# Kernel tuning notes

Hardware: AMD Instinct MI355X
Metric: run time of the kernel (lower is better)

## Reference

```python
import jax, jax.numpy as jnp
import numpy as np

N, E = 50000, 800000
D, H, C, ED = 128, 8, 16, 4  # embed_dim, heads, head_dim, edge_dim


def _add_self_loops(edge_index, ea, n):
    # PyG add_self_loops with fill_value='mean': self-loop edge_attr is the
    # mean of incoming edge attributes per destination node (0 if none).
    src, dst = edge_index[0], edge_index[1]
    deg = jax.ops.segment_sum(jnp.ones((src.shape[0],), ea.dtype), dst, num_segments=n)
    loop_ea = jax.ops.segment_sum(ea, dst, num_segments=n) / jnp.maximum(deg, 1.0)[:, None]
    ar = jnp.arange(n, dtype=src.dtype)
    return (jnp.concatenate([src, ar]), jnp.concatenate([dst, ar]),
            jnp.concatenate([ea, loop_ea], axis=0))


def _gatv2(x, src, dst, ea, Wl, bl, Wr, br, We, att, bias, concat):
    n = x.shape[0]
    xl = (x @ Wl + bl).reshape(n, H, C)   # lin_l -> messages (source)
    xr = (x @ Wr + br).reshape(n, H, C)   # lin_r -> target
    e = (ea @ We).reshape(-1, H, C)       # lin_edge (no bias in PyG)
    m = jax.nn.leaky_relu(xl[src] + xr[dst] + e, negative_slope=0.2)  # [Etot,H,C]
    alpha = jnp.einsum('ehc,hc->eh', m, att)
    amax = jax.ops.segment_max(alpha, dst, num_segments=n)   # every node has a self loop
    ex = jnp.exp(alpha - amax[dst])
    den = jax.ops.segment_sum(ex, dst, num_segments=n)
    a = ex / den[dst]                                        # segment softmax over dst
    out = jax.ops.segment_sum(xl[src] * a[:, :, None], dst, num_segments=n)  # [N,H,C]
    out = out.reshape(n, H * C) if concat else out.mean(axis=1)
    return out + bias


def _ln(h, g, b):
    mu = h.mean(-1, keepdims=True)
    var = jnp.var(h, axis=-1, keepdims=True)
    return (h - mu) / jnp.sqrt(var + 1e-5) * g + b


def setup_inputs() -> dict:
    key = jax.random.key(0)
    ks = jax.random.split(key, 32)
    s = 0.05
    inp = {
        'x': jax.random.normal(ks[0], (N, D), jnp.float32),
        'edge_index': jax.random.randint(ks[1], (2, E), 0, N, jnp.int32),
        'edge_attr': jax.random.normal(ks[2], (E, ED), jnp.float32),
    }
    dims = [(D, H * C), (H * C, H * C), (H * C, C)]  # (in_dim, bias_dim per layer)
    k = 3
    for i, (din, bdim) in enumerate(dims):
        inp[f'Wl{i}'] = jax.random.normal(ks[k], (din, H * C), jnp.float32) * s; k += 1
        inp[f'bl{i}'] = jnp.zeros((H * C,), jnp.float32)
        inp[f'Wr{i}'] = jax.random.normal(ks[k], (din, H * C), jnp.float32) * s; k += 1
        inp[f'br{i}'] = jnp.zeros((H * C,), jnp.float32)
        inp[f'We{i}'] = jax.random.normal(ks[k], (ED, H * C), jnp.float32) * s; k += 1
        inp[f'att{i}'] = jax.random.normal(ks[k], (H, C), jnp.float32) * s; k += 1
        inp[f'b{i}'] = jnp.zeros((bdim,), jnp.float32)
        inp[f'g{i}'] = jnp.ones((bdim,), jnp.float32)
        inp[f'be{i}'] = jnp.zeros((bdim,), jnp.float32)
    inp['Wout'] = jax.random.normal(ks[k], (C, D), jnp.float32) * s
    inp['bout'] = jnp.zeros((D,), jnp.float32)
    return inp


def reference(x, edge_index, edge_attr,
              Wl0, bl0, Wr0, br0, We0, att0, b0, g0, be0,
              Wl1, bl1, Wr1, br1, We1, att1, b1, g1, be1,
              Wl2, bl2, Wr2, br2, We2, att2, b2, g2, be2,
              Wout, bout):
    n = x.shape[0]
    src, dst, ea = _add_self_loops(edge_index, edge_attr, n)
    layers = [
        (Wl0, bl0, Wr0, br0, We0, att0, b0, g0, be0, True),
        (Wl1, bl1, Wr1, br1, We1, att1, b1, g1, be1, True),
        (Wl2, bl2, Wr2, br2, We2, att2, b2, g2, be2, False),
    ]
    for (Wl, bl, Wr, br, We, att, bias, g, be, concat) in layers:
        h = _gatv2(x, src, dst, ea, Wl, bl, Wr, br, We, att, bias, concat)
        h = jax.nn.elu(h)
        h = _ln(h, g, be)
        if h.shape == x.shape:  # residual (layers 0,1)
            h = h + x
        x = h
    return x @ Wout + bout
```

## Files before the change

kernel.cpp:

```cpp
#include <hip/hip_runtime.h>
#include <hip/hip_bf16.h>

#define ND 128
#define NH 8
#define NC 16

typedef float v2f __attribute__((ext_vector_type(2)));

static inline size_t alignup(size_t x){ return (x + 255) & ~size_t(255); }

__device__ __forceinline__ ushort f2bf(float f){
    __hip_bfloat16 h = __float2bfloat16(f);
    return *reinterpret_cast<ushort*>(&h);
}

__device__ __forceinline__ v2f unpack_bf2(uint u){
    v2f r;
    r.x = __uint_as_float(u << 16);
    r.y = __uint_as_float(u & 0xffff0000u);
    return r;
}

__device__ __forceinline__ v2f lrelu2(v2f z){
    v2f s = z * 0.2f;
    v2f r;
    r.x = fmaxf(z.x, s.x);
    r.y = fmaxf(z.y, s.y);
    return r;
}

__device__ __forceinline__ float hred8(float x){
    int y;
    y = __builtin_amdgcn_mov_dpp(__float_as_int(x), 0xB1, 0xF, 0xF, true);
    x += __int_as_float(y);
    y = __builtin_amdgcn_mov_dpp(__float_as_int(x), 0x4E, 0xF, 0xF, true);
    x += __int_as_float(y);
    y = __builtin_amdgcn_mov_dpp(__float_as_int(x), 0x141, 0xF, 0xF, true);
    x += __int_as_float(y);
    return x;
}


__global__ void hist_kernel(const int* __restrict__ dsts, int* __restrict__ deg, int E)
{
    int e = blockIdx.x * blockDim.x + threadIdx.x;
    if (e >= E) return;
    atomicAdd(&deg[dsts[e]], 1);
}

__global__ __launch_bounds__(1024) void scan_kernel(const int* __restrict__ deg,
                                                    int* __restrict__ rowstart, int n)
{
    __shared__ int wsum[16];
    int tid = threadIdx.x;
    int lane = tid & 63, wid = tid >> 6;
    int carry = 0;
    for (int base = 0; base < n; base += 1024) {
        int idx = base + tid;
        int v = (idx < n) ? ((deg[idx] + 3) & ~3) : 0;
        int s = v;
        #pragma unroll
        for (int o = 1; o < 64; o <<= 1) {
            int t = __shfl_up(s, o);
            if (lane >= o) s += t;
        }
        if (lane == 63) wsum[wid] = s;
        __syncthreads();
        int off = 0;
        #pragma unroll
        for (int w = 0; w < 16; ++w) {
            int ws_ = wsum[w];
            if (w < wid) off += ws_;
        }
        int total = 0;
        #pragma unroll
        for (int w = 0; w < 16; ++w) total += wsum[w];
        if (idx < n) rowstart[idx] = carry + off + (s - v);
        carry += total;
        __syncthreads();
    }
    if (tid == 0) rowstart[n] = carry;
}

__global__ void scatter_kernel(const int* __restrict__ srcs, const int* __restrict__ dsts,
                               const float4* __restrict__ ea4,
                               const int* __restrict__ rowstart, int* __restrict__ cursor,
                               int* __restrict__ srcb_sorted, float4* __restrict__ ea_sorted, int E)
{
    int e = blockIdx.x * blockDim.x + threadIdx.x;
    if (e >= E) return;
    int d = dsts[e];
    int pos = rowstart[d] + atomicAdd(&cursor[d], 1);
    srcb_sorted[pos] = srcs[e] << 8;
    ea_sorted[pos] = ea4[e];
}

__global__ void padfill_kernel(const int* __restrict__ rowstart, const int* __restrict__ deg,
                               int* __restrict__ srcb_sorted, float4* __restrict__ ea_sorted, int n)
{
    int v = blockIdx.x * blockDim.x + threadIdx.x;
    if (v < n) {
        int d = deg[v];
        int p = rowstart[v] + d;
        int pe = rowstart[v] + ((d + 3) & ~3);
        for (; p < pe; ++p) {
            srcb_sorted[p] = 0;
            ea_sorted[p] = make_float4(0.f, 0.f, 0.f, 0.f);
        }
    } else if (v < n + 64) {
        int p = rowstart[n] + (v - n);
        srcb_sorted[p] = 0;
        ea_sorted[p] = make_float4(0.f, 0.f, 0.f, 0.f);
    }
}

__global__ void easum_kernel(const int* __restrict__ rowstart, const int* __restrict__ deg,
                             const float4* __restrict__ ea_sorted, float4* __restrict__ easum, int n)
{
    int v = blockIdx.x * blockDim.x + threadIdx.x;
    if (v >= n) return;
    int p0 = rowstart[v], d = deg[v];
    float sx = 0.f, sy = 0.f, sz = 0.f, sw = 0.f;
    for (int p = p0; p < p0 + d; ++p) {
        float4 a = ea_sorted[p];
        sx += a.x; sy += a.y; sz += a.z; sw += a.w;
    }
    float inv = 1.0f / (float)(d > 0 ? d : 1);
    easum[v] = make_float4(sx * inv, sy * inv, sz * inv, sw * inv);
}


__global__ __launch_bounds__(256) void gemm_xw2(const float* __restrict__ X,
                                                const float* __restrict__ Wl,
                                                const float* __restrict__ bl,
                                                const float* __restrict__ Wr,
                                                const float* __restrict__ br,
                                                ushort* __restrict__ XLB,
                                                ushort* __restrict__ XRB, int nrows)
{
    __shared__ float xs[64][128];
    int tid = threadIdx.x;
    int row0 = blockIdx.x * 64;

    const float4* X4 = (const float4*)X;
    float4* xs4 = (float4*)xs;
    #pragma unroll
    for (int i = tid; i < 64*32; i += 256) {
        int r = i >> 5;
        float4 v = make_float4(0.f, 0.f, 0.f, 0.f);
        if (row0 + r < nrows) v = X4[(size_t)(row0 + r) * 32 + (i & 31)];
        xs4[i] = v;
    }
    __syncthreads();

    int cg = tid & 31;
    int rg = (tid >> 5) * 8;
    v2f al0[8], al1[8], ar0[8], ar1[8];
    float4 blv = ((const float4*)bl)[cg];
    float4 brv = ((const float4*)br)[cg];
    #pragma unroll
    for (int r = 0; r < 8; r++) {
        al0[r] = (v2f){blv.x, blv.y}; al1[r] = (v2f){blv.z, blv.w};
        ar0[r] = (v2f){brv.x, brv.y}; ar1[r] = (v2f){brv.z, brv.w};
    }

    #pragma unroll 2
    for (int k = 0; k < 128; k++) {
        float4 wl = ((const float4*)(Wl + (size_t)k * 128))[cg];
        float4 wr = ((const float4*)(Wr + (size_t)k * 128))[cg];
        v2f wl01 = (v2f){wl.x, wl.y}, wl23 = (v2f){wl.z, wl.w};
        v2f wr01 = (v2f){wr.x, wr.y}, wr23 = (v2f){wr.z, wr.w};
        #pragma unroll
        for (int r = 0; r < 8; r++) {
            float xv = xs[rg + r][k];
            v2f xv2 = (v2f){xv, xv};
            al0[r] += xv2 * wl01;
            al1[r] += xv2 * wl23;
            ar0[r] += xv2 * wr01;
            ar1[r] += xv2 * wr23;
        }
    }

    #pragma unroll
    for (int r = 0; r < 8; r++) {
        int row = row0 + rg + r;
        if (row < nrows) {
            ushort4 ol, orr;
            ol.x = f2bf(al0[r].x); ol.y = f2bf(al0[r].y);
            ol.z = f2bf(al1[r].x); ol.w = f2bf(al1[r].y);
            orr.x = f2bf(ar0[r].x); orr.y = f2bf(ar0[r].y);
            orr.z = f2bf(ar1[r].x); orr.w = f2bf(ar1[r].y);
            ((ushort4*)XLB)[(size_t)row * 32 + cg] = ol;
            ((ushort4*)XRB)[(size_t)row * 32 + cg] = orr;
        }
    }
}


__device__ __forceinline__ void gat_wave(
    int dstv, int t,
    const uint* __restrict__ xl_u, const uint* __restrict__ xr_u,
    const int* __restrict__ rowstart, const int* __restrict__ deg,
    const int* __restrict__ srcb_sorted, const float4* __restrict__ ea_sorted,
    const float4* __restrict__ easum,
    const float* __restrict__ We, const float* __restrict__ att,
    v2f& r_out, float& l_out)
{
    v2f we0  = ((const v2f*)(We))[t];
    v2f we1  = ((const v2f*)(We + ND))[t];
    v2f we2  = ((const v2f*)(We + 2*ND))[t];
    v2f we3  = ((const v2f*)(We + 3*ND))[t];
    v2f attv = ((const v2f*)att)[t] * 1.44269504f;
    v2f xrv  = unpack_bf2(xr_u[(((uint)dstv) << 6) + t]);

    int p0 = __builtin_amdgcn_readfirstlane(rowstart[dstv]);
    int dv = __builtin_amdgcn_readfirstlane(deg[dstv]);
    int nb = (dv + 3) >> 2;

    uint xsw = xl_u[(((uint)dstv) << 6) + t];

    const int* sp = srcb_sorted + p0;
    const float4* ep = ea_sorted + p0;
    const char* xlc = (const char*)xl_u;
    uint t4 = (uint)t * 4u;

    v2f a = {0.f, 0.f};
    float lsum = 0.f;

    int4 sA = *(const int4*)(sp);
    uint xA0 = *(const uint*)(xlc + ((uint)sA.x + t4));
    uint xA1 = *(const uint*)(xlc + ((uint)sA.y + t4));
    uint xA2 = *(const uint*)(xlc + ((uint)sA.z + t4));
    uint xA3 = *(const uint*)(xlc + ((uint)sA.w + t4));
    int4 sB = *(const int4*)(sp + 4);
    uint xB0 = *(const uint*)(xlc + ((uint)sB.x + t4));
    uint xB1 = *(const uint*)(xlc + ((uint)sB.y + t4));
    uint xB2 = *(const uint*)(xlc + ((uint)sB.z + t4));
    uint xB3 = *(const uint*)(xlc + ((uint)sB.w + t4));
    int4 sC = *(const int4*)(sp + 8);

    for (int ib = 0; ib < nb; ++ib) {
        uint xC0 = *(const uint*)(xlc + ((uint)sC.x + t4));
        uint xC1 = *(const uint*)(xlc + ((uint)sC.y + t4));
        uint xC2 = *(const uint*)(xlc + ((uint)sC.z + t4));
        uint xC3 = *(const uint*)(xlc + ((uint)sC.w + t4));
        int4 sD = *(const int4*)(sp + ib*4 + 12);
        float4 ea0 = ep[ib*4];
        float4 ea1 = ep[ib*4 + 1];
        float4 ea2 = ep[ib*4 + 2];
        float4 ea3 = ep[ib*4 + 3];

        v2f b0 = xrv + we0*ea0.x + we1*ea0.y + we2*ea0.z + we3*ea0.w;
        v2f b1 = xrv + we0*ea1.x + we1*ea1.y + we2*ea1.z + we3*ea1.w;
        v2f b2 = xrv + we0*ea2.x + we1*ea2.y + we2*ea2.z + we3*ea2.w;
        v2f b3 = xrv + we0*ea3.x + we1*ea3.y + we2*ea3.z + we3*ea3.w;

        v2f x0 = unpack_bf2(xA0);
        v2f x1 = unpack_bf2(xA1);
        v2f x2 = unpack_bf2(xA2);
        v2f x3 = unpack_bf2(xA3);

        v2f l0 = lrelu2(x0 + b0);
        v2f l1 = lrelu2(x1 + b1);
        v2f l2 = lrelu2(x2 + b2);
        v2f l3 = lrelu2(x3 + b3);

        v2f q0 = l0 * attv;
        v2f q1 = l1 * attv;
        v2f q2 = l2 * attv;
        v2f q3 = l3 * attv;
        float pt0 = q0.x + q0.y;
        float pt1 = q1.x + q1.y;
        float pt2 = q2.x + q2.y;
        float pt3 = q3.x + q3.y;

        if (ib == nb - 1) {
            int live = dv - ib*4;
            pt1 = (live > 1) ? pt1 : -1e30f;
            pt2 = (live > 2) ? pt2 : -1e30f;
            pt3 = (live > 3) ? pt3 : -1e30f;
        }

        float al0 = hred8(pt0);
        float al1 = hred8(pt1);
        float al2 = hred8(pt2);
        float al3 = hred8(pt3);

        float pe0 = exp2f(al0);
        float pe1 = exp2f(al1);
        float pe2 = exp2f(al2);
        float pe3 = exp2f(al3);
        lsum += (pe0 + pe1) + (pe2 + pe3);
        a += x0 * pe0;
        a += x1 * pe1;
        a += x2 * pe2;
        a += x3 * pe3;

        xA0 = xB0; xA1 = xB1; xA2 = xB2; xA3 = xB3;
        xB0 = xC0; xB1 = xC1; xB2 = xC2; xB3 = xC3;
        sC = sD;
    }

    float4 em = easum[dstv];
    v2f xs = unpack_bf2(xsw);
    v2f bs = xrv + we0*em.x + we1*em.y + we2*em.z + we3*em.w;
    v2f ls = lrelu2(xs + bs);
    v2f qs = ls * attv;
    float al = hred8(qs.x + qs.y);
    float pe = exp2f(al);
    l_out = lsum + pe;
    r_out = a + xs * pe;
}

__global__ __launch_bounds__(256) void attn_concat(
    const ushort* __restrict__ xlb, const ushort* __restrict__ xrb,
    const float* __restrict__ xin,
    const int* __restrict__ rowstart, const int* __restrict__ deg,
    const int* __restrict__ srcb_sorted, const float4* __restrict__ ea_sorted,
    const float4* __restrict__ easum,
    const float* __restrict__ We, const float* __restrict__ att,
    const float* __restrict__ bias, const float* __restrict__ g, const float* __restrict__ be,
    float* __restrict__ out, int n)
{
    int wid = threadIdx.x >> 6;
    int t = threadIdx.x & 63;
    int dstv = blockIdx.x * 4 + wid;
    if (dstv >= n) return;

    v2f av; float l;
    gat_wave(dstv, t, (const uint*)xlb, (const uint*)xrb, rowstart, deg, srcb_sorted,
             ea_sorted, easum, We, att, av, l);

    v2f bv = ((const v2f*)bias)[t];
    float linv = 1.0f / l;
    v2f h = av * linv + bv;
    h.x = h.x > 0.f ? h.x : (__expf(h.x) - 1.0f);
    h.y = h.y > 0.f ? h.y : (__expf(h.y) - 1.0f);

    float ss = h.x + h.y, qq = h.x*h.x + h.y*h.y;
    #pragma unroll
    for (int o = 1; o < 64; o <<= 1) { ss += __shfl_xor(ss, o); qq += __shfl_xor(qq, o); }
    float mu = ss * (1.0f / ND);
    float var = qq * (1.0f / ND) - mu * mu;
    float rstd = rsqrtf(var + 1e-5f);

    v2f gv  = ((const v2f*)g)[t];
    v2f bev = ((const v2f*)be)[t];
    v2f xiv = ((const v2f*)(xin + (size_t)dstv * ND))[t];
    v2f o2 = (h - mu) * rstd * gv + bev + xiv;
    ((v2f*)(out + (size_t)dstv * ND))[t] = o2;
}

__global__ __launch_bounds__(256) void attn_final(
    const ushort* __restrict__ xlb, const ushort* __restrict__ xrb,
    const int* __restrict__ rowstart, const int* __restrict__ deg,
    const int* __restrict__ srcb_sorted, const float4* __restrict__ ea_sorted,
    const float4* __restrict__ easum,
    const float* __restrict__ We, const float* __restrict__ att,
    const float* __restrict__ b2, const float* __restrict__ g2, const float* __restrict__ be2,
    const float* __restrict__ Wout, const float* __restrict__ bout,
    float* __restrict__ out, int n)
{
    __shared__ float h16s[4][16];
    int wid = threadIdx.x >> 6;
    int t = threadIdx.x & 63;
    int dstv = blockIdx.x * 4 + wid;
    if (dstv >= n) return;

    v2f av; float l;
    gat_wave(dstv, t, (const uint*)xlb, (const uint*)xrb, rowstart, deg, srcb_sorted,
             ea_sorted, easum, We, att, av, l);
    float linv = 1.0f / l;
    float v0 = av.x * linv, v1 = av.y * linv;

    #pragma unroll
    for (int o = 8; o < 64; o <<= 1) { v0 += __shfl_xor(v0, o); v1 += __shfl_xor(v1, o); }
    int cc = t & 7;
    float2 b2v = ((const float2*)b2)[cc];
    v0 = v0 * (1.0f / NH) + b2v.x;
    v1 = v1 * (1.0f / NH) + b2v.y;
    v0 = v0 > 0.f ? v0 : (__expf(v0) - 1.0f);
    v1 = v1 > 0.f ? v1 : (__expf(v1) - 1.0f);

    float ss = v0 + v1, qq = v0*v0 + v1*v1;
    #pragma unroll
    for (int o = 1; o < 8; o <<= 1) { ss += __shfl_xor(ss, o); qq += __shfl_xor(qq, o); }
    float mu = ss * (1.0f / NC);
    float var = qq * (1.0f / NC) - mu * mu;
    float rstd = rsqrtf(var + 1e-5f);
    float2 g2v = ((const float2*)g2)[cc];
    float2 be2v = ((const float2*)be2)[cc];
    float t0 = (v0 - mu) * rstd * g2v.x + be2v.x;
    float t1 = (v1 - mu) * rstd * g2v.y + be2v.y;

    if (t < 8) { h16s[wid][2*t] = t0; h16s[wid][2*t + 1] = t1; }

    float2 ov = ((const float2*)bout)[t];
    #pragma unroll
    for (int k = 0; k < NC; k++) {
        float hk = h16s[wid][k];
        float2 wv = ((const float2*)Wout)[k * 64 + t];
        ov.x = fmaf(hk, wv.x, ov.x);
        ov.y = fmaf(hk, wv.y, ov.y);
    }
    ((float2*)(out + (size_t)dstv * ND))[t] = ov;
}


extern "C" void kernel_launch(void* const* d_in, const int* in_sizes, int n_in,
                              void* d_out, int out_size, void* d_ws, size_t ws_size,
                              hipStream_t stream)
{
    const float* x_in = (const float*)d_in[0];
    const int*   ei   = (const int*)d_in[1];
    const float* ea   = (const float*)d_in[2];
    const int N = in_sizes[0] / ND;
    const int E = in_sizes[1] / 2;
    const int* srcs = ei;
    const int* dsts = ei + E;
    const float4* ea4 = (const float4*)ea;

    const float *Wl[3], *bl[3], *Wr[3], *br[3], *We[3], *att[3], *bb[3], *gg[3], *be[3];
    for (int l = 0; l < 3; l++) {
        int b = 3 + 9 * l;
        Wl[l]  = (const float*)d_in[b + 0];
        bl[l]  = (const float*)d_in[b + 1];
        Wr[l]  = (const float*)d_in[b + 2];
        br[l]  = (const float*)d_in[b + 3];
        We[l]  = (const float*)d_in[b + 4];
        att[l] = (const float*)d_in[b + 5];
        bb[l]  = (const float*)d_in[b + 6];
        gg[l]  = (const float*)d_in[b + 7];
        be[l]  = (const float*)d_in[b + 8];
    }
    const float* Wout = (const float*)d_in[30];
    const float* bout = (const float*)d_in[31];

    const size_t EP = (size_t)E + 3 * (size_t)N + 80;

    char* ws = (char*)d_ws;
    size_t off = 0;
    int* deg        = (int*)(ws + off);      off = alignup(off + (size_t)N * 4);
    int* cursor     = (int*)(ws + off);      off = alignup(off + (size_t)N * 4);
    size_t zero_bytes = off;
    int* rowstart   = (int*)(ws + off);      off = alignup(off + (size_t)(N + 1) * 4);
    int* srcb_sorted = (int*)(ws + off);     off = alignup(off + EP * 4);
    float4* ea_sorted = (float4*)(ws + off); off = alignup(off + EP * 16);
    float4* easum   = (float4*)(ws + off);   off = alignup(off + (size_t)N * 16);
    ushort* xlb     = (ushort*)(ws + off);   off = alignup(off + (size_t)N * ND * 2);
    ushort* xrb     = (ushort*)(ws + off);   off = alignup(off + (size_t)N * ND * 2);
    float* xa       = (float*)(ws + off);    off = alignup(off + (size_t)N * ND * 4);
    float* xb       = (float*)d_out;

    hipMemsetAsync(d_ws, 0, zero_bytes, stream);

    int ethreads = 256;
    int eblocks = (E + ethreads - 1) / ethreads;
    hist_kernel<<<eblocks, ethreads, 0, stream>>>(dsts, deg, E);
    scan_kernel<<<1, 1024, 0, stream>>>(deg, rowstart, N);
    padfill_kernel<<<(N + 64 + 255) / 256, 256, 0, stream>>>(rowstart, deg, srcb_sorted, ea_sorted, N);
    scatter_kernel<<<eblocks, ethreads, 0, stream>>>(srcs, dsts, ea4, rowstart, cursor,
                                                     srcb_sorted, ea_sorted, E);
    easum_kernel<<<(N + 255) / 256, 256, 0, stream>>>(rowstart, deg, ea_sorted, easum, N);

    int gblocks = (N + 63) / 64;
    int ablocks = (N + 3) / 4;

    gemm_xw2<<<gblocks, 256, 0, stream>>>(x_in, Wl[0], bl[0], Wr[0], br[0], xlb, xrb, N);
    attn_concat<<<ablocks, 256, 0, stream>>>(xlb, xrb, x_in, rowstart, deg, srcb_sorted, ea_sorted,
                                             easum, We[0], att[0], bb[0], gg[0], be[0], xa, N);
    gemm_xw2<<<gblocks, 256, 0, stream>>>(xa, Wl[1], bl[1], Wr[1], br[1], xlb, xrb, N);
    attn_concat<<<ablocks, 256, 0, stream>>>(xlb, xrb, xa, rowstart, deg, srcb_sorted, ea_sorted,
                                             easum, We[1], att[1], bb[1], gg[1], be[1], xb, N);
    gemm_xw2<<<gblocks, 256, 0, stream>>>(xb, Wl[2], bl[2], Wr[2], br[2], xlb, xrb, N);
    attn_final<<<ablocks, 256, 0, stream>>>(xlb, xrb, rowstart, deg, srcb_sorted, ea_sorted,
                                            easum, We[2], att[2], bb[2], gg[2], be[2],
                                            Wout, bout, (float*)d_out, N);
}
```

Measured before the change: 480.5 us.

## Store edge attrs as bf16, deepen gather prefetch, stage weights in LDS, vectorize scan

Sorted edge attributes are packed as bf16 pairs (8 bytes instead of 16 per edge), which cuts edge-attribute traffic in the attention kernels and in easum. The attention loop's source-feature prefetch goes from two to three blocks ahead, and edge attributes are loaded one block ahead. The GEMM stages Wl/Wr in LDS in 16-row tiles with register double-buffering instead of reading weights from global memory each k. The scan now handles four elements per thread. The cost is bf16 rounding of edge attributes and higher register pressure in the attention loop.

```diff
diff --git a/kernel.cpp b/kernel.cpp
--- a/kernel.cpp
+++ b/kernel.cpp
@@ -55,10 +55,19 @@
     int tid = threadIdx.x;
     int lane = tid & 63, wid = tid >> 6;
     int carry = 0;
-    for (int base = 0; base < n; base += 1024) {
-        int idx = base + tid;
-        int v = (idx < n) ? ((deg[idx] + 3) & ~3) : 0;
-        int s = v;
+    for (int base = 0; base < n; base += 4096) {
+        int idx = base + tid * 4;
+        int4 d = make_int4(0, 0, 0, 0);
+        if (idx + 3 < n) d = *(const int4*)(deg + idx);
+        else {
+            if (idx < n)     d.x = deg[idx];
+            if (idx + 1 < n) d.y = deg[idx + 1];
+            if (idx + 2 < n) d.z = deg[idx + 2];
+        }
+        int p0 = (d.x + 3) & ~3, p1 = (d.y + 3) & ~3;
+        int p2 = (d.z + 3) & ~3, p3 = (d.w + 3) & ~3;
+        int tsum = p0 + p1 + p2 + p3;
+        int s = tsum;
         #pragma unroll
         for (int o = 1; o < 64; o <<= 1) {
             int t = __shfl_up(s, o);
@@ -66,7 +75,7 @@
         }
         if (lane == 63) wsum[wid] = s;
         __syncthreads();
-        int off = 0;
+        int off = carry;
         #pragma unroll
         for (int w = 0; w < 16; ++w) {
             int ws_ = wsum[w];
@@ -75,7 +84,11 @@
         int total = 0;
         #pragma unroll
         for (int w = 0; w < 16; ++w) total += wsum[w];
-        if (idx < n) rowstart[idx] = carry + off + (s - v);
+        int excl = off + (s - tsum);
+        if (idx < n)     rowstart[idx]     = excl;
+        if (idx + 1 < n) rowstart[idx + 1] = excl + p0;
+        if (idx + 2 < n) rowstart[idx + 2] = excl + p0 + p1;
+        if (idx + 3 < n) rowstart[idx + 3] = excl + p0 + p1 + p2;
         carry += total;
         __syncthreads();
     }
@@ -85,18 +98,22 @@
 __global__ void scatter_kernel(const int* __restrict__ srcs, const int* __restrict__ dsts,
                                const float4* __restrict__ ea4,
                                const int* __restrict__ rowstart, int* __restrict__ cursor,
-                               int* __restrict__ srcb_sorted, float4* __restrict__ ea_sorted, int E)
+                               int* __restrict__ srcb_sorted, uint2* __restrict__ eab_sorted, int E)
 {
     int e = blockIdx.x * blockDim.x + threadIdx.x;
     if (e >= E) return;
     int d = dsts[e];
     int pos = rowstart[d] + atomicAdd(&cursor[d], 1);
     srcb_sorted[pos] = srcs[e] << 8;
-    ea_sorted[pos] = ea4[e];
+    float4 a = ea4[e];
+    uint2 p;
+    p.x = (uint)f2bf(a.x) | ((uint)f2bf(a.y) << 16);
+    p.y = (uint)f2bf(a.z) | ((uint)f2bf(a.w) << 16);
+    eab_sorted[pos] = p;
 }
 
 __global__ void padfill_kernel(const int* __restrict__ rowstart, const int* __restrict__ deg,
-                               int* __restrict__ srcb_sorted, float4* __restrict__ ea_sorted, int n)
+                               int* __restrict__ srcb_sorted, uint2* __restrict__ eab_sorted, int n)
 {
     int v = blockIdx.x * blockDim.x + threadIdx.x;
     if (v < n) {
@@ -105,25 +122,28 @@
         int pe = rowstart[v] + ((d + 3) & ~3);
         for (; p < pe; ++p) {
             srcb_sorted[p] = 0;
-            ea_sorted[p] = make_float4(0.f, 0.f, 0.f, 0.f);
+            eab_sorted[p] = make_uint2(0u, 0u);
         }
     } else if (v < n + 64) {
         int p = rowstart[n] + (v - n);
         srcb_sorted[p] = 0;
-        ea_sorted[p] = make_float4(0.f, 0.f, 0.f, 0.f);
+        eab_sorted[p] = make_uint2(0u, 0u);
     }
 }
 
 __global__ void easum_kernel(const int* __restrict__ rowstart, const int* __restrict__ deg,
-                             const float4* __restrict__ ea_sorted, float4* __restrict__ easum, int n)
+                             const uint2* __restrict__ eab_sorted, float4* __restrict__ easum, int n)
 {
     int v = blockIdx.x * blockDim.x + threadIdx.x;
     if (v >= n) return;
     int p0 = rowstart[v], d = deg[v];
     float sx = 0.f, sy = 0.f, sz = 0.f, sw = 0.f;
     for (int p = p0; p < p0 + d; ++p) {
-        float4 a = ea_sorted[p];
-        sx += a.x; sy += a.y; sz += a.z; sw += a.w;
+        uint2 a = eab_sorted[p];
+        sx += __uint_as_float(a.x << 16);
+        sy += __uint_as_float(a.x & 0xffff0000u);
+        sz += __uint_as_float(a.y << 16);
+        sw += __uint_as_float(a.y & 0xffff0000u);
     }
     float inv = 1.0f / (float)(d > 0 ? d : 1);
     easum[v] = make_float4(sx * inv, sy * inv, sz * inv, sw * inv);
@@ -139,6 +159,8 @@
                                                 ushort* __restrict__ XRB, int nrows)
 {
     __shared__ float xs[64][128];
+    __shared__ float wls[16][128];
+    __shared__ float wrs[16][128];
     int tid = threadIdx.x;
     int row0 = blockIdx.x * 64;
 
@@ -151,7 +173,11 @@
         if (row0 + r < nrows) v = X4[(size_t)(row0 + r) * 32 + (i & 31)];
         xs4[i] = v;
     }
-    __syncthreads();
+
+    const float4* Wl4 = (const float4*)Wl;
+    const float4* Wr4 = (const float4*)Wr;
+    float4 pa0 = Wl4[tid], pa1 = Wl4[tid + 256];
+    float4 pb0 = Wr4[tid], pb1 = Wr4[tid + 256];
 
     int cg = tid & 31;
     int rg = (tid >> 5) * 8;
@@ -164,20 +190,31 @@
         ar0[r] = (v2f){brv.x, brv.y}; ar1[r] = (v2f){brv.z, brv.w};
     }
 
-    #pragma unroll 2
-    for (int k = 0; k < 128; k++) {
-        float4 wl = ((const float4*)(Wl + (size_t)k * 128))[cg];
-        float4 wr = ((const float4*)(Wr + (size_t)k * 128))[cg];
-        v2f wl01 = (v2f){wl.x, wl.y}, wl23 = (v2f){wl.z, wl.w};
-        v2f wr01 = (v2f){wr.x, wr.y}, wr23 = (v2f){wr.z, wr.w};
+    for (int kt = 0; kt < 128; kt += 16) {
+        __syncthreads();
+        ((float4*)wls)[tid] = pa0; ((float4*)wls)[tid + 256] = pa1;
+        ((float4*)wrs)[tid] = pb0; ((float4*)wrs)[tid + 256] = pb1;
+        __syncthreads();
+        if (kt + 16 < 128) {
+            int base = (kt + 16) * 32;
+            pa0 = Wl4[base + tid]; pa1 = Wl4[base + tid + 256];
+            pb0 = Wr4[base + tid]; pb1 = Wr4[base + tid + 256];
+        }
         #pragma unroll
-        for (int r = 0; r < 8; r++) {
-            float xv = xs[rg + r][k];
-            v2f xv2 = (v2f){xv, xv};
-            al0[r] += xv2 * wl01;
-            al1[r] += xv2 * wl23;
-            ar0[r] += xv2 * wr01;
-            ar1[r] += xv2 * wr23;
+        for (int kk = 0; kk < 16; kk++) {
+            float4 wl = ((const float4*)&wls[kk][0])[cg];
+            float4 wr = ((const float4*)&wrs[kk][0])[cg];
+            v2f wl01 = (v2f){wl.x, wl.y}, wl23 = (v2f){wl.z, wl.w};
+            v2f wr01 = (v2f){wr.x, wr.y}, wr23 = (v2f){wr.z, wr.w};
+            #pragma unroll
+            for (int r = 0; r < 8; r++) {
+                float xv = xs[rg + r][kt + kk];
+                v2f xv2 = (v2f){xv, xv};
+                al0[r] += xv2 * wl01;
+                al1[r] += xv2 * wl23;
+                ar0[r] += xv2 * wr01;
+                ar1[r] += xv2 * wr23;
+            }
         }
     }
 
@@ -201,7 +238,7 @@
     int dstv, int t,
     const uint* __restrict__ xl_u, const uint* __restrict__ xr_u,
     const int* __restrict__ rowstart, const int* __restrict__ deg,
-    const int* __restrict__ srcb_sorted, const float4* __restrict__ ea_sorted,
+    const int* __restrict__ srcb_sorted, const uint2* __restrict__ eab_sorted,
     const float4* __restrict__ easum,
     const float* __restrict__ We, const float* __restrict__ att,
     v2f& r_out, float& l_out)
@@ -220,40 +257,54 @@
     uint xsw = xl_u[(((uint)dstv) << 6) + t];
 
     const int* sp = srcb_sorted + p0;
-    const float4* ep = ea_sorted + p0;
+    const uint4* ebp = (const uint4*)(eab_sorted + p0);
     const char* xlc = (const char*)xl_u;
     uint t4 = (uint)t * 4u;
 
     v2f a = {0.f, 0.f};
     float lsum = 0.f;
 
-    int4 sA = *(const int4*)(sp);
-    uint xA0 = *(const uint*)(xlc + ((uint)sA.x + t4));
-    uint xA1 = *(const uint*)(xlc + ((uint)sA.y + t4));
-    uint xA2 = *(const uint*)(xlc + ((uint)sA.z + t4));
-    uint xA3 = *(const uint*)(xlc + ((uint)sA.w + t4));
-    int4 sB = *(const int4*)(sp + 4);
-    uint xB0 = *(const uint*)(xlc + ((uint)sB.x + t4));
-    uint xB1 = *(const uint*)(xlc + ((uint)sB.y + t4));
-    uint xB2 = *(const uint*)(xlc + ((uint)sB.z + t4));
-    uint xB3 = *(const uint*)(xlc + ((uint)sB.w + t4));
-    int4 sC = *(const int4*)(sp + 8);
+    int4 s0 = *(const int4*)(sp);
+    uint xA0 = *(const uint*)(xlc + ((uint)s0.x + t4));
+    uint xA1 = *(const uint*)(xlc + ((uint)s0.y + t4));
+    uint xA2 = *(const uint*)(xlc + ((uint)s0.z + t4));
+    uint xA3 = *(const uint*)(xlc + ((uint)s0.w + t4));
+    int4 s1 = *(const int4*)(sp + 4);
+    uint xB0 = *(const uint*)(xlc + ((uint)s1.x + t4));
+    uint xB1 = *(const uint*)(xlc + ((uint)s1.y + t4));
+    uint xB2 = *(const uint*)(xlc + ((uint)s1.z + t4));
+    uint xB3 = *(const uint*)(xlc + ((uint)s1.w + t4));
+    int4 s2 = *(const int4*)(sp + 8);
+    uint xC0 = *(const uint*)(xlc + ((uint)s2.x + t4));
+    uint xC1 = *(const uint*)(xlc + ((uint)s2.y + t4));
+    uint xC2 = *(const uint*)(xlc + ((uint)s2.z + t4));
+    uint xC3 = *(const uint*)(xlc + ((uint)s2.w + t4));
+    int4 s3 = *(const int4*)(sp + 12);
+    uint4 eA = ebp[0];
+    uint4 eB = ebp[1];
 
     for (int ib = 0; ib < nb; ++ib) {
-        uint xC0 = *(const uint*)(xlc + ((uint)sC.x + t4));
-        uint xC1 = *(const uint*)(xlc + ((uint)sC.y + t4));
-        uint xC2 = *(const uint*)(xlc + ((uint)sC.z + t4));
-        uint xC3 = *(const uint*)(xlc + ((uint)sC.w + t4));
-        int4 sD = *(const int4*)(sp + ib*4 + 12);
-        float4 ea0 = ep[ib*4];
-        float4 ea1 = ep[ib*4 + 1];
-        float4 ea2 = ep[ib*4 + 2];
-        float4 ea3 = ep[ib*4 + 3];
-
-        v2f b0 = xrv + we0*ea0.x + we1*ea0.y + we2*ea0.z + we3*ea0.w;
-        v2f b1 = xrv + we0*ea1.x + we1*ea1.y + we2*ea1.z + we3*ea1.w;
-        v2f b2 = xrv + we0*ea2.x + we1*ea2.y + we2*ea2.z + we3*ea2.w;
-        v2f b3 = xrv + we0*ea3.x + we1*ea3.y + we2*ea3.z + we3*ea3.w;
+        uint xD0 = *(const uint*)(xlc + ((uint)s3.x + t4));
+        uint xD1 = *(const uint*)(xlc + ((uint)s3.y + t4));
+        uint xD2 = *(const uint*)(xlc + ((uint)s3.z + t4));
+        uint xD3 = *(const uint*)(xlc + ((uint)s3.w + t4));
+        int4 s4 = *(const int4*)(sp + ib*4 + 16);
+        uint4 eNA = ebp[(ib + 1) * 2];
+        uint4 eNB = ebp[(ib + 1) * 2 + 1];
+
+        float e0x = __uint_as_float(eA.x << 16), e0y = __uint_as_float(eA.x & 0xffff0000u);
+        float e0z = __uint_as_float(eA.y << 16), e0w = __uint_as_float(eA.y & 0xffff0000u);
+        float e1x = __uint_as_float(eA.z << 16), e1y = __uint_as_float(eA.z & 0xffff0000u);
+        float e1z = __uint_as_float(eA.w << 16), e1w = __uint_as_float(eA.w & 0xffff0000u);
+        float e2x = __uint_as_float(eB.x << 16), e2y = __uint_as_float(eB.x & 0xffff0000u);
+        float e2z = __uint_as_float(eB.y << 16), e2w = __uint_as_float(eB.y & 0xffff0000u);
+        float e3x = __uint_as_float(eB.z << 16), e3y = __uint_as_float(eB.z & 0xffff0000u);
+        float e3z = __uint_as_float(eB.w << 16), e3w = __uint_as_float(eB.w & 0xffff0000u);
+
+        v2f b0 = xrv + we0*e0x + we1*e0y + we2*e0z + we3*e0w;
+        v2f b1 = xrv + we0*e1x + we1*e1y + we2*e1z + we3*e1w;
+        v2f b2 = xrv + we0*e2x + we1*e2y + we2*e2z + we3*e2w;
+        v2f b3 = xrv + we0*e3x + we1*e3y + we2*e3z + we3*e3w;
 
         v2f x0 = unpack_bf2(xA0);
         v2f x1 = unpack_bf2(xA1);
@@ -298,7 +349,9 @@
 
         xA0 = xB0; xA1 = xB1; xA2 = xB2; xA3 = xB3;
         xB0 = xC0; xB1 = xC1; xB2 = xC2; xB3 = xC3;
-        sC = sD;
+        xC0 = xD0; xC1 = xD1; xC2 = xD2; xC3 = xD3;
+        s3 = s4;
+        eA = eNA; eB = eNB;
     }
 
     float4 em = easum[dstv];
@@ -316,7 +369,7 @@
     const ushort* __restrict__ xlb, const ushort* __restrict__ xrb,
     const float* __restrict__ xin,
     const int* __restrict__ rowstart, const int* __restrict__ deg,
-    const int* __restrict__ srcb_sorted, const float4* __restrict__ ea_sorted,
+    const int* __restrict__ srcb_sorted, const uint2* __restrict__ eab_sorted,
     const float4* __restrict__ easum,
     const float* __restrict__ We, const float* __restrict__ att,
     const float* __restrict__ bias, const float* __restrict__ g, const float* __restrict__ be,
@@ -329,7 +382,7 @@
 
     v2f av; float l;
     gat_wave(dstv, t, (const uint*)xlb, (const uint*)xrb, rowstart, deg, srcb_sorted,
-             ea_sorted, easum, We, att, av, l);
+             eab_sorted, easum, We, att, av, l);
 
     v2f bv = ((const v2f*)bias)[t];
     float linv = 1.0f / l;
@@ -354,7 +407,7 @@
 __global__ __launch_bounds__(256) void attn_final(
     const ushort* __restrict__ xlb, const ushort* __restrict__ xrb,
     const int* __restrict__ rowstart, const int* __restrict__ deg,
-    const int* __restrict__ srcb_sorted, const float4* __restrict__ ea_sorted,
+    const int* __restrict__ srcb_sorted, const uint2* __restrict__ eab_sorted,
     const float4* __restrict__ easum,
     const float* __restrict__ We, const float* __restrict__ att,
     const float* __restrict__ b2, const float* __restrict__ g2, const float* __restrict__ be2,
@@ -369,7 +422,7 @@
 
     v2f av; float l;
     gat_wave(dstv, t, (const uint*)xlb, (const uint*)xrb, rowstart, deg, srcb_sorted,
-             ea_sorted, easum, We, att, av, l);
+             eab_sorted, easum, We, att, av, l);
     float linv = 1.0f / l;
     float v0 = av.x * linv, v1 = av.y * linv;
 
@@ -436,7 +489,7 @@
     const float* Wout = (const float*)d_in[30];
     const float* bout = (const float*)d_in[31];
 
-    const size_t EP = (size_t)E + 3 * (size_t)N + 80;
+    const size_t EP = (size_t)E + 3 * (size_t)N + 96;
 
     char* ws = (char*)d_ws;
     size_t off = 0;
@@ -445,7 +498,7 @@
     size_t zero_bytes = off;
     int* rowstart   = (int*)(ws + off);      off = alignup(off + (size_t)(N + 1) * 4);
     int* srcb_sorted = (int*)(ws + off);     off = alignup(off + EP * 4);
-    float4* ea_sorted = (float4*)(ws + off); off = alignup(off + EP * 16);
+    uint2* eab_sorted = (uint2*)(ws + off);  off = alignup(off + EP * 8);
     float4* easum   = (float4*)(ws + off);   off = alignup(off + (size_t)N * 16);
     ushort* xlb     = (ushort*)(ws + off);   off = alignup(off + (size_t)N * ND * 2);
     ushort* xrb     = (ushort*)(ws + off);   off = alignup(off + (size_t)N * ND * 2);
@@ -458,22 +511,22 @@
     int eblocks = (E + ethreads - 1) / ethreads;
     hist_kernel<<<eblocks, ethreads, 0, stream>>>(dsts, deg, E);
     scan_kernel<<<1, 1024, 0, stream>>>(deg, rowstart, N);
-    padfill_kernel<<<(N + 64 + 255) / 256, 256, 0, stream>>>(rowstart, deg, srcb_sorted, ea_sorted, N);
+    padfill_kernel<<<(N + 64 + 255) / 256, 256, 0, stream>>>(rowstart, deg, srcb_sorted, eab_sorted, N);
     scatter_kernel<<<eblocks, ethreads, 0, stream>>>(srcs, dsts, ea4, rowstart, cursor,
-                                                     srcb_sorted, ea_sorted, E);
-    easum_kernel<<<(N + 255) / 256, 256, 0, stream>>>(rowstart, deg, ea_sorted, easum, N);
+                                                     srcb_sorted, eab_sorted, E);
+    easum_kernel<<<(N + 255) / 256, 256, 0, stream>>>(rowstart, deg, eab_sorted, easum, N);
 
     int gblocks = (N + 63) / 64;
     int ablocks = (N + 3) / 4;
 
     gemm_xw2<<<gblocks, 256, 0, stream>>>(x_in, Wl[0], bl[0], Wr[0], br[0], xlb, xrb, N);
-    attn_concat<<<ablocks, 256, 0, stream>>>(xlb, xrb, x_in, rowstart, deg, srcb_sorted, ea_sorted,
+    attn_concat<<<ablocks, 256, 0, stream>>>(xlb, xrb, x_in, rowstart, deg, srcb_sorted, eab_sorted,
                                              easum, We[0], att[0], bb[0], gg[0], be[0], xa, N);
     gemm_xw2<<<gblocks, 256, 0, stream>>>(xa, Wl[1], bl[1], Wr[1], br[1], xlb, xrb, N);
-    attn_concat<<<ablocks, 256, 0, stream>>>(xlb, xrb, xa, rowstart, deg, srcb_sorted, ea_sorted,
+    attn_concat<<<ablocks, 256, 0, stream>>>(xlb, xrb, xa, rowstart, deg, srcb_sorted, eab_sorted,
                                              easum, We[1], att[1], bb[1], gg[1], be[1], xb, N);
     gemm_xw2<<<gblocks, 256, 0, stream>>>(xb, Wl[2], bl[2], Wr[2], br[2], xlb, xrb, N);
-    attn_final<<<ablocks, 256, 0, stream>>>(xlb, xrb, rowstart, deg, srcb_sorted, ea_sorted,
+    attn_final<<<ablocks, 256, 0, stream>>>(xlb, xrb, rowstart, deg, srcb_sorted, eab_sorted,
                                             easum, We[2], att[2], bb[2], gg[2], be[2],
                                             Wout, bout, (float*)d_out, N);
 }
```

Result: faster. 459.5 us (-4.4%).
